# Optimization experiments

Hardware: AMD Instinct MI355X
Metric: run time of the kernel (lower is better)

The kernel has to match this reference:

```python
import jax, jax.numpy as jnp
import numpy as np
import math, itertools

# ---- hyperparams (from init_kwargs) ----
S_SCALE = 30.0
MARGIN = 0.2
ALPHA = 0.1
N_CLASS = 200000
EMB_DIM = 192
B, N, S = 64, 3, 3  # batch, embedding slots, speakers per utterance (S <= N)

COS_M = math.cos(MARGIN)
SIN_M = math.sin(MARGIN)
TH = math.cos(math.pi - MARGIN)
MM = math.sin(math.pi - MARGIN) * MARGIN

# all permutations of N slots (exact Hungarian for square S==N cost matrices)
PERMS = np.array(list(itertools.permutations(range(N))), dtype=np.int32)  # [P, N]


def setup_inputs() -> dict:
    key = jax.random.key(0)
    k1, k2, k3, k4 = jax.random.split(key, 4)
    pred_embs = jax.random.normal(k1, (B, N, EMB_DIM), jnp.float32)
    pred_ps = jax.random.uniform(k2, (B, N + 1), jnp.float32)
    gt_labels = jax.random.randint(k3, (B, S), 0, N_CLASS, dtype=jnp.int32)
    weight = jax.random.normal(k4, (N_CLASS, EMB_DIM), jnp.float32)
    return {"pred_embs": pred_embs, "pred_ps": pred_ps,
            "gt_labels": gt_labels, "weight": weight}


def _l2norm(x, axis=-1, eps=1e-6):
    n = jnp.sqrt(jnp.sum(x * x, axis=axis, keepdims=True))
    return x / jnp.maximum(n, eps)


def _cost_matrix(pred_embs, weight, gt_labels):
    """Batched ArcFace CE cost for every (speaker, slot) pair -> [B, S, N]."""
    x = _l2norm(pred_embs)                     # [B, N, D]
    Wn = _l2norm(weight)                       # [C, D]
    cosine = jnp.einsum('bnd,cd->bnc', x, Wn)  # [B, N, C]
    cosine = jnp.clip(cosine, -1.0 + 1e-7, 1.0 - 1e-7)
    lse_all = jax.scipy.special.logsumexp(S_SCALE * cosine, axis=-1)  # [B, N]

    # gather cosine at the S target labels: [B, N, S]
    cos_l = jnp.take_along_axis(cosine, gt_labels[:, None, :], axis=2)
    sin_l = jnp.sqrt(jnp.clip(1.0 - cos_l * cos_l, 1e-7, None))
    phi = cos_l * COS_M - sin_l * SIN_M
    phi = jnp.where(cos_l > TH, phi, cos_l - MM)

    # CE with label-logit replaced by phi: lse over modified row, stable
    lse = lse_all[:, :, None]
    lse_mod = lse + jnp.log1p(jnp.exp(S_SCALE * phi - lse) - jnp.exp(S_SCALE * cos_l - lse))
    ce = lse_mod - S_SCALE * phi               # [B, N, S]
    return jnp.transpose(ce, (0, 2, 1))        # [B, S, N]  (C[i, n] as in torch)


def reference(pred_embs, pred_ps, gt_labels, weight):
    C = _cost_matrix(pred_embs, weight, gt_labels)       # [B, S, N]
    rows = np.arange(S)[None, :]                         # [1, S]
    sel = C[:, rows, PERMS]                              # [B, P, S] costs per perm
    perm_cost = sel.sum(axis=-1)                         # [B, P]
    best = jnp.argmin(jax.lax.stop_gradient(perm_cost), axis=1)  # detached assignment
    matched = jnp.take_along_axis(sel, best[:, None, None], axis=1)[:, 0, :]  # [B, S]
    L_spk = matched.mean(axis=1)                         # [B]

    p = jnp.clip(pred_ps, 1e-6, 1.0 - 1e-6)              # [B, N+1]
    # S <= N branch: valid = p[:S], stop = p[S]  (S=3 so no S==1/2 overrides)
    L_cnt = -(jnp.log1p(-p[:, :S]).sum(axis=1) + jnp.log(p[:, S])) / (S + 1)

    L_spk_total = L_spk.mean()
    L_cnt_total = L_cnt.mean()
    L_total = L_spk_total + ALPHA * L_cnt_total
    return (L_total, L_spk_total, L_cnt_total)
```

## Files before the change

### kernel.cpp

```cpp
#include <hip/hip_runtime.h>
#include <hip/hip_bf16.h>
#include <math.h>

#define N_CLASS 200000
#define DIM     192
#define BATCH   64
#define NSLOT   3
#define M_ROWS  192
#define GRID_M  1024

#define S_SCALE 30.0f
#define COS_M   0.9800665778412416f
#define SIN_M   0.19866933079506122f
#define TH_C    (-0.9800665778412416f)
#define MM_C    0.039733866159012245f

typedef __attribute__((ext_vector_type(8))) short bf16x8;
typedef __attribute__((ext_vector_type(4))) float f32x4;

__device__ __forceinline__ float wave_reduce_sum(float v) {
#pragma unroll
    for (int o = 32; o > 0; o >>= 1) v += __shfl_xor(v, o, 64);
    return v;
}

__device__ __forceinline__ unsigned short f2bf(float f) {
    union { __hip_bfloat16 h; unsigned short u; } v;
    v.h = __float2bfloat16(f);
    return v.u;
}

__device__ __forceinline__ bf16x8 pack8(float4 a, float4 b) {
    bf16x8 r;
    r[0] = (short)f2bf(a.x); r[1] = (short)f2bf(a.y);
    r[2] = (short)f2bf(a.z); r[3] = (short)f2bf(a.w);
    r[4] = (short)f2bf(b.x); r[5] = (short)f2bf(b.y);
    r[6] = (short)f2bf(b.z); r[7] = (short)f2bf(b.w);
    return r;
}

__global__ void k_normalize(const float* __restrict__ pe,
                            float* __restrict__ xn, unsigned short* __restrict__ xbf) {
    int r = blockIdx.x;
    int l = threadIdx.x;
    float v0 = pe[r * DIM + l];
    float v1 = pe[r * DIM + l + 64];
    float v2 = pe[r * DIM + l + 128];
    float ss = wave_reduce_sum(v0 * v0 + v1 * v1 + v2 * v2);
    float rn = 1.0f / fmaxf(sqrtf(ss), 1e-6f);
    float a0 = v0 * rn, a1 = v1 * rn, a2 = v2 * rn;
    xn[r * DIM + l]       = a0;
    xn[r * DIM + l + 64]  = a1;
    xn[r * DIM + l + 128] = a2;
    xbf[r * DIM + l]       = f2bf(a0);
    xbf[r * DIM + l + 64]  = f2bf(a1);
    xbf[r * DIM + l + 128] = f2bf(a2);
}

__global__ void k_gtcos(const float* __restrict__ weight, const int* __restrict__ gt,
                        const float* __restrict__ xn, float* __restrict__ cosl) {
    int i = blockIdx.x;
    int b = i / NSLOT, s = i - b * NSLOT;
    int l = threadIdx.x;
    int lab = gt[b * NSLOT + s];
    const float* w = weight + (long)lab * DIM;
    float w0 = w[l], w1 = w[l + 64], w2 = w[l + 128];
    float ss = wave_reduce_sum(w0 * w0 + w1 * w1 + w2 * w2);
    float rn = 1.0f / fmaxf(sqrtf(ss), 1e-6f);
    for (int n = 0; n < NSLOT; ++n) {
        const float* x = xn + (b * NSLOT + n) * DIM;
        float d = wave_reduce_sum(w0 * x[l] + w1 * x[l + 64] + w2 * x[l + 128]);
        float c = fminf(fmaxf(d * rn, -1.0f + 1e-7f), 1.0f - 1e-7f);
        if (l == 0) cosl[(b * NSLOT + n) * NSLOT + s] = c;
    }
}

__global__ __launch_bounds__(256, 2)
void k_main(const float* __restrict__ weight,
            const unsigned short* __restrict__ xbf,
            float* __restrict__ partials) {
    __shared__ __align__(16) float4 wtile[2][48 * 17 + 1];

    const int tid  = threadIdx.x;
    const int lane = tid & 63;
    const int rg   = tid >> 6;
    const int lr   = lane & 15;
    const int q    = lane >> 4;
    const int bid  = blockIdx.x;

    const int ntile = 12 + (bid < 212 ? 1 : 0);

    bf16x8 areg[3][6];
#pragma unroll
    for (int t = 0; t < 3; ++t) {
        const unsigned short* xp = xbf + (rg * 48 + t * 16 + lr) * DIM + q * 8;
#pragma unroll
        for (int s = 0; s < 6; ++s)
            areg[t][s] = *reinterpret_cast<const bf16x8*>(xp + s * 32);
    }

    int wr0, wr1, wr2;
    {
        int f0 = tid,       r0 = f0 / 48, c0 = f0 - r0 * 48;
        int f1 = tid + 256, r1 = f1 / 48, c1 = f1 - r1 * 48;
        int f2 = tid + 512, r2 = f2 / 48, c2 = f2 - r2 * 48;
        wr0 = c0 * 17 + r0; wr1 = c1 * 17 + r1; wr2 = c2 * 17 + r2;
    }

    const float4* gW = reinterpret_cast<const float4*>(weight) + (long)bid * 768 + tid;
    const long tstep4 = (long)GRID_M * 768;

    float4 st0 = gW[0], st1 = gW[256], st2 = gW[512];
    gW += tstep4;

    f32x4 acc[3];
#pragma unroll
    for (int t = 0; t < 3; ++t) acc[t] = (f32x4){0.f, 0.f, 0.f, 0.f};
    float rs[3][4];
#pragma unroll
    for (int t = 0; t < 3; ++t)
#pragma unroll
        for (int r = 0; r < 4; ++r) rs[t][r] = 0.f;

    const int rbase = 34 * q + lr;

#pragma unroll 1
    for (int j = 0; j < ntile; ++j) {
        float4* buf = &wtile[j & 1][0];
        buf[wr0] = st0; buf[wr1] = st1; buf[wr2] = st2;
        asm volatile("s_waitcnt lgkmcnt(0)" ::: "memory");
        __builtin_amdgcn_s_barrier();
        __builtin_amdgcn_sched_barrier(0);
        if (j + 1 < ntile) {
            st0 = gW[0]; st1 = gW[256]; st2 = gW[512];
            gW += tstep4;
        }
        float sq = 0.f;
#pragma unroll
        for (int s = 0; s < 6; ++s) {
            float4 wv1 = buf[136 * s + rbase];
            float4 wv2 = buf[136 * s + rbase + 17];
            sq += wv1.x*wv1.x + wv1.y*wv1.y + wv1.z*wv1.z + wv1.w*wv1.w
                + wv2.x*wv2.x + wv2.y*wv2.y + wv2.z*wv2.z + wv2.w*wv2.w;
            bf16x8 bb = pack8(wv1, wv2);
            acc[0] = __builtin_amdgcn_mfma_f32_16x16x32_bf16(areg[0][s], bb, acc[0], 0, 0, 0);
            acc[1] = __builtin_amdgcn_mfma_f32_16x16x32_bf16(areg[1][s], bb, acc[1], 0, 0, 0);
            acc[2] = __builtin_amdgcn_mfma_f32_16x16x32_bf16(areg[2][s], bb, acc[2], 0, 0, 0);
        }
        sq += __shfl_xor(sq, 16); sq += __shfl_xor(sq, 32);
        float rn = 1.0f / fmaxf(sqrtf(sq), 1e-6f);
#pragma unroll
        for (int t = 0; t < 3; ++t)
#pragma unroll
            for (int r = 0; r < 4; ++r) {
                float c = fminf(fmaxf(acc[t][r] * rn, -1.0f + 1e-7f), 1.0f - 1e-7f);
                rs[t][r] += __expf(S_SCALE * c - 30.0f);
                acc[t][r] = 0.f;
            }
    }

#pragma unroll
    for (int t = 0; t < 3; ++t)
#pragma unroll
        for (int r = 0; r < 4; ++r) {
            float v = rs[t][r];
            v += __shfl_xor(v, 1); v += __shfl_xor(v, 2);
            v += __shfl_xor(v, 4); v += __shfl_xor(v, 8);
            if (lr == 0)
                partials[(long)bid * M_ROWS + (rg * 48 + t * 16 + q * 4 + r)] = v;
        }
}

__global__ void k_reduce(const float* __restrict__ partials, float* __restrict__ sum_exp) {
    int r = blockIdx.x;
    float s = 0.0f;
    for (int i = threadIdx.x; i < GRID_M; i += 256)
        s += partials[(long)i * M_ROWS + r];
    s = wave_reduce_sum(s);
    __shared__ float wsm[4];
    int wid = threadIdx.x >> 6;
    if ((threadIdx.x & 63) == 0) wsm[wid] = s;
    __syncthreads();
    if (threadIdx.x == 0) sum_exp[r] = wsm[0] + wsm[1] + wsm[2] + wsm[3];
}

__global__ void k_final(const float* __restrict__ sum_exp, const float* __restrict__ cosl,
                        const float* __restrict__ pred_ps, float* __restrict__ out) {
    int b = threadIdx.x;
    const int perms[6][3] = {{0,1,2},{0,2,1},{1,0,2},{1,2,0},{2,0,1},{2,1,0}};
    float ce[3][3];
#pragma unroll
    for (int n = 0; n < 3; ++n) {
        float lse = 30.0f + logf(sum_exp[b * 3 + n]);
#pragma unroll
        for (int s = 0; s < 3; ++s) {
            float c  = cosl[(b * 3 + n) * 3 + s];
            float sl = sqrtf(fmaxf(1.0f - c * c, 1e-7f));
            float phi = c * COS_M - sl * SIN_M;
            phi = (c > TH_C) ? phi : (c - MM_C);
            float lm = lse + log1pf(expf(S_SCALE * phi - lse) - expf(S_SCALE * c - lse));
            ce[n][s] = lm - S_SCALE * phi;
        }
    }
    float best = 1e30f;
    int bp = 0;
#pragma unroll
    for (int p = 0; p < 6; ++p) {
        float cost = ce[perms[p][0]][0] + ce[perms[p][1]][1] + ce[perms[p][2]][2];
        if (cost < best) { best = cost; bp = p; }
    }
    float lspk = (ce[perms[bp][0]][0] + ce[perms[bp][1]][1] + ce[perms[bp][2]][2]) / 3.0f;

    float p0 = fminf(fmaxf(pred_ps[b * 4 + 0], 1e-6f), 1.0f - 1e-6f);
    float p1 = fminf(fmaxf(pred_ps[b * 4 + 1], 1e-6f), 1.0f - 1e-6f);
    float p2 = fminf(fmaxf(pred_ps[b * 4 + 2], 1e-6f), 1.0f - 1e-6f);
    float p3 = fminf(fmaxf(pred_ps[b * 4 + 3], 1e-6f), 1.0f - 1e-6f);
    float lcnt = -(log1pf(-p0) + log1pf(-p1) + log1pf(-p2) + logf(p3)) * 0.25f;

    float ts  = wave_reduce_sum(lspk) / 64.0f;
    float tcn = wave_reduce_sum(lcnt) / 64.0f;
    if (b == 0) {
        out[0] = ts + 0.1f * tcn;
        out[1] = ts;
        out[2] = tcn;
    }
}

extern "C" void kernel_launch(void* const* d_in, const int* in_sizes, int n_in,
                              void* d_out, int out_size, void* d_ws, size_t ws_size,
                              hipStream_t stream) {
    const float* pred_embs = (const float*)d_in[0];
    const float* pred_ps   = (const float*)d_in[1];
    const int*   gt_labels = (const int*)d_in[2];
    const float* weight    = (const float*)d_in[3];
    float* out = (float*)d_out;
    char*  ws  = (char*)d_ws;

    float*          xn       = (float*)(ws);
    unsigned short* xbf      = (unsigned short*)(ws + 147456);
    float*          cosl     = (float*)(ws + 221184);
    float*          sum_exp  = (float*)(ws + 223488);
    float*          partials = (float*)(ws + 224256);

    k_normalize<<<M_ROWS, 64, 0, stream>>>(pred_embs, xn, xbf);
    k_main<<<GRID_M, 256, 0, stream>>>(weight, xbf, partials);
    k_gtcos<<<BATCH * NSLOT, 64, 0, stream>>>(weight, gt_labels, xn, cosl);
    k_reduce<<<M_ROWS, 256, 0, stream>>>(partials, sum_exp);
    k_final<<<1, 64, 0, stream>>>(sum_exp, cosl, pred_ps, out);
}
```

Before: 57.28 us.

## Deepen weight prefetch to two tiles and transpose partials for coalesced reduce

The main loop now holds two register-staged weight tiles in flight (sa/sb), unrolled in pairs with a tail for odd counts, so global loads run two iterations ahead of compute and hide more latency. The partials buffer is transposed to [row][block], which lets k_reduce read each row with one coalesced float4 per thread instead of strided scalar loads. The cost is extra VGPRs for the second staging set, which could lower occupancy, and k_reduce now assumes GRID_M equals 4×256.

```diff
diff --git a/kernel.cpp b/kernel.cpp
--- a/kernel.cpp
+++ b/kernel.cpp
@@ -110,7 +110,9 @@
     const float4* gW = reinterpret_cast<const float4*>(weight) + (long)bid * 768 + tid;
     const long tstep4 = (long)GRID_M * 768;
 
-    float4 st0 = gW[0], st1 = gW[256], st2 = gW[512];
+    float4 sa0 = gW[0], sa1 = gW[256], sa2 = gW[512];
+    gW += tstep4;
+    float4 sb0 = gW[0], sb1 = gW[256], sb2 = gW[512];
     gW += tstep4;
 
     f32x4 acc[3];
@@ -124,40 +126,69 @@
 
     const int rbase = 34 * q + lr;
 
+#define COMPUTE(bufp)                                                          \
+    {                                                                          \
+        float sq = 0.f;                                                        \
+        _Pragma("unroll")                                                      \
+        for (int s = 0; s < 6; ++s) {                                          \
+            float4 wv1 = (bufp)[136 * s + rbase];                              \
+            float4 wv2 = (bufp)[136 * s + rbase + 17];                         \
+            sq += wv1.x*wv1.x + wv1.y*wv1.y + wv1.z*wv1.z + wv1.w*wv1.w        \
+                + wv2.x*wv2.x + wv2.y*wv2.y + wv2.z*wv2.z + wv2.w*wv2.w;       \
+            bf16x8 bb = pack8(wv1, wv2);                                       \
+            acc[0] = __builtin_amdgcn_mfma_f32_16x16x32_bf16(areg[0][s], bb, acc[0], 0, 0, 0); \
+            acc[1] = __builtin_amdgcn_mfma_f32_16x16x32_bf16(areg[1][s], bb, acc[1], 0, 0, 0); \
+            acc[2] = __builtin_amdgcn_mfma_f32_16x16x32_bf16(areg[2][s], bb, acc[2], 0, 0, 0); \
+        }                                                                      \
+        sq += __shfl_xor(sq, 16); sq += __shfl_xor(sq, 32);                    \
+        float rn = 1.0f / fmaxf(sqrtf(sq), 1e-6f);                             \
+        _Pragma("unroll")                                                      \
+        for (int t = 0; t < 3; ++t)                                            \
+            _Pragma("unroll")                                                  \
+            for (int r = 0; r < 4; ++r) {                                      \
+                float c = fminf(fmaxf(acc[t][r] * rn, -1.0f + 1e-7f), 1.0f - 1e-7f); \
+                rs[t][r] += __expf(S_SCALE * c - 30.0f);                       \
+                acc[t][r] = 0.f;                                               \
+            }                                                                  \
+    }
+
+    const int npair = ntile >> 1;
 #pragma unroll 1
-    for (int j = 0; j < ntile; ++j) {
-        float4* buf = &wtile[j & 1][0];
-        buf[wr0] = st0; buf[wr1] = st1; buf[wr2] = st2;
+    for (int p = 0; p < npair; ++p) {
+        {
+            float4* buf = &wtile[0][0];
+            buf[wr0] = sa0; buf[wr1] = sa1; buf[wr2] = sa2;
+            asm volatile("s_waitcnt lgkmcnt(0)" ::: "memory");
+            __builtin_amdgcn_s_barrier();
+            __builtin_amdgcn_sched_barrier(0);
+            if (2 * p + 2 < ntile) {
+                sa0 = gW[0]; sa1 = gW[256]; sa2 = gW[512];
+                gW += tstep4;
+            }
+            COMPUTE(buf)
+        }
+        {
+            float4* buf = &wtile[1][0];
+            buf[wr0] = sb0; buf[wr1] = sb1; buf[wr2] = sb2;
+            asm volatile("s_waitcnt lgkmcnt(0)" ::: "memory");
+            __builtin_amdgcn_s_barrier();
+            __builtin_amdgcn_sched_barrier(0);
+            if (2 * p + 3 < ntile) {
+                sb0 = gW[0]; sb1 = gW[256]; sb2 = gW[512];
+                gW += tstep4;
+            }
+            COMPUTE(buf)
+        }
+    }
+    if (ntile & 1) {
+        float4* buf = &wtile[0][0];
+        buf[wr0] = sa0; buf[wr1] = sa1; buf[wr2] = sa2;
         asm volatile("s_waitcnt lgkmcnt(0)" ::: "memory");
         __builtin_amdgcn_s_barrier();
         __builtin_amdgcn_sched_barrier(0);
-        if (j + 1 < ntile) {
-            st0 = gW[0]; st1 = gW[256]; st2 = gW[512];
-            gW += tstep4;
-        }
-        float sq = 0.f;
-#pragma unroll
-        for (int s = 0; s < 6; ++s) {
-            float4 wv1 = buf[136 * s + rbase];
-            float4 wv2 = buf[136 * s + rbase + 17];
-            sq += wv1.x*wv1.x + wv1.y*wv1.y + wv1.z*wv1.z + wv1.w*wv1.w
-                + wv2.x*wv2.x + wv2.y*wv2.y + wv2.z*wv2.z + wv2.w*wv2.w;
-            bf16x8 bb = pack8(wv1, wv2);
-            acc[0] = __builtin_amdgcn_mfma_f32_16x16x32_bf16(areg[0][s], bb, acc[0], 0, 0, 0);
-            acc[1] = __builtin_amdgcn_mfma_f32_16x16x32_bf16(areg[1][s], bb, acc[1], 0, 0, 0);
-            acc[2] = __builtin_amdgcn_mfma_f32_16x16x32_bf16(areg[2][s], bb, acc[2], 0, 0, 0);
-        }
-        sq += __shfl_xor(sq, 16); sq += __shfl_xor(sq, 32);
-        float rn = 1.0f / fmaxf(sqrtf(sq), 1e-6f);
-#pragma unroll
-        for (int t = 0; t < 3; ++t)
-#pragma unroll
-            for (int r = 0; r < 4; ++r) {
-                float c = fminf(fmaxf(acc[t][r] * rn, -1.0f + 1e-7f), 1.0f - 1e-7f);
-                rs[t][r] += __expf(S_SCALE * c - 30.0f);
-                acc[t][r] = 0.f;
-            }
-    }
+        COMPUTE(buf)
+    }
+#undef COMPUTE
 
 #pragma unroll
     for (int t = 0; t < 3; ++t)
@@ -167,15 +198,14 @@
             v += __shfl_xor(v, 1); v += __shfl_xor(v, 2);
             v += __shfl_xor(v, 4); v += __shfl_xor(v, 8);
             if (lr == 0)
-                partials[(long)bid * M_ROWS + (rg * 48 + t * 16 + q * 4 + r)] = v;
+                partials[(long)(rg * 48 + t * 16 + q * 4 + r) * GRID_M + bid] = v;
         }
 }
 
 __global__ void k_reduce(const float* __restrict__ partials, float* __restrict__ sum_exp) {
     int r = blockIdx.x;
-    float s = 0.0f;
-    for (int i = threadIdx.x; i < GRID_M; i += 256)
-        s += partials[(long)i * M_ROWS + r];
+    float4 v = reinterpret_cast<const float4*>(partials + (long)r * GRID_M)[threadIdx.x];
+    float s = v.x + v.y + v.z + v.w;
     s = wave_reduce_sum(s);
     __shared__ float wsm[4];
     int wid = threadIdx.x >> 6;
```

Measured after the change: 56.43 us. Within noise of the previous version (-1.5%).
